# Kernel tuning notes

Hardware: AMD Instinct MI355X
Metric: run time of the kernel (lower is better)

## Reference

```python
import jax, jax.numpy as jnp
import numpy as np
from jax.scipy.special import logsumexp

N, K, D = 131072, 256, 32


def setup_inputs() -> dict:
    key = jax.random.key(0)
    k1, k2, k3 = jax.random.split(key, 3)
    points = jax.random.normal(k1, (N, D), dtype=jnp.float32)
    centers = jax.random.uniform(k2, (K, D), dtype=jnp.float32)
    # well-conditioned inverse-sqrt covariances (original used 15*I; scaled to
    # avoid float32 overflow in sqrt(det(covs_inv)) for D=32)
    covs_inv_sqrt = (0.5 * jnp.broadcast_to(jnp.eye(D, dtype=jnp.float32), (K, D, D))
                     + 0.02 * jax.random.normal(k3, (K, D, D), dtype=jnp.float32))
    weights = jnp.ones((K,), dtype=jnp.float32)
    threshold = jnp.zeros((1,), dtype=jnp.float32)
    return {"points": points, "centers": centers,
            "covs_inv_sqrt": covs_inv_sqrt, "weights": weights,
            "threshold": threshold}


def reference(points, centers, covs_inv_sqrt, weights, threshold):
    # refresh(): equal_clusters=True branch
    w = jnp.abs(weights)
    center_prs = w / (w.sum() + 1e-30)                       # [K]
    covs_inv = jnp.einsum('kde,kfe->kdf', covs_inv_sqrt, covs_inv_sqrt)  # [K,D,D]
    coefs = center_prs * jnp.sqrt(jnp.linalg.det(covs_inv))  # [K]

    # pairwise weighted sqdist: q_ij = (x_i - c_j)^T A_j (x_i - c_j)
    B = covs_inv.reshape(K, D * D)                           # [K, D*D]
    X2 = (points[:, :, None] * points[:, None, :]).reshape(N, D * D)  # [N, D*D]
    t_xAx = X2 @ B.T                                         # [N, K]
    m = jnp.einsum('kde,ke->kd', covs_inv, centers)          # A_j c_j, [K,D]
    t_xAc = points @ m.T                                     # [N, K]
    t_cAc = jnp.einsum('kd,kd->k', m, centers)               # [K]
    d_ij = -0.5 * (t_xAx - 2.0 * t_xAc + t_cAc[None, :])     # [N, K]

    # weighted logsumexp over centers, then subtract threshold
    ll = logsumexp(d_ij, axis=1, b=coefs[None, :])           # [N]
    return ll[:, None] - threshold[0]                        # [N, 1]
```

## Files before the change

kernel.cpp:

```cpp
#include <hip/hip_runtime.h>
#include <math.h>

#define NPTS 131072
#define KCOMP 256
#define DIM 32
#define KF 576
#define NREAL 560
#define PSIF_BYTES 294912
#define WS_NEED (PSIF_BYTES + KCOMP * 4)

typedef __attribute__((ext_vector_type(8))) short short8;
typedef __attribute__((ext_vector_type(16))) float f32x16;

__device__ __forceinline__ unsigned short f2bf(float v) {
    unsigned u = __float_as_uint(v);
    u += 0x7fffu + ((u >> 16) & 1u);
    return (unsigned short)(u >> 16);
}

__device__ __forceinline__ unsigned pkbf(float lo, float hi) {
#if __has_builtin(__builtin_amdgcn_perm)
    const unsigned a = __float_as_uint(hi) + 0x8000u;
    const unsigned b = __float_as_uint(lo) + 0x8000u;
    return __builtin_amdgcn_perm(a, b, 0x07060302u);
#else
    return (unsigned)f2bf(lo) | ((unsigned)f2bf(hi) << 16);
#endif
}

__device__ __forceinline__ void dma16(const uint4* g, uint4* s) {
    __builtin_amdgcn_global_load_lds(
        (const __attribute__((address_space(1))) void*)g,
        (__attribute__((address_space(3))) void*)s, 16, 0, 0);
}

__device__ __forceinline__ void barrier_lds_only() {
    asm volatile("s_waitcnt lgkmcnt(0)\ns_barrier" ::: "memory");
}

constexpr int PfxT(int d) { return 32 * d - (d * (d - 1)) / 2; }
constexpr int rowT(int p) { int d = 0; while (d < 31 && PfxT(d + 1) <= p) ++d; return d; }
constexpr int colT(int p) { return rowT(p) + (p - PfxT(rowT(p))); }

template<int P, int J>
__device__ __forceinline__ float genOne(const float (&x)[DIM]) {
    constexpr int p = P + J;
    if constexpr (p >= NREAL) {
        return 0.f;
    } else if constexpr (p >= 528) {
        return x[p - 528];
    } else {
        constexpr int d = rowT(p);
        constexpr int f = colT(p);
        static_assert(d >= 0 && d < 32 && f >= d && f < 32, "bad feature map");
        return x[d] * x[f];
    }
}

__global__ __launch_bounds__(256) void gmm_pre(
    const float* __restrict__ S,
    const float* __restrict__ centers,
    const float* __restrict__ weights,
    unsigned short* __restrict__ PsiF,
    float* __restrict__ kc2)
{
    __shared__ float Sl[DIM][DIM + 1];
    __shared__ float As[DIM][DIM + 1];
    __shared__ float cl[DIM], ml[DIM];
    __shared__ float red[256];

    const int k = blockIdx.x, tid = threadIdx.x;

    for (int idx = tid; idx < DIM * DIM; idx += 256)
        Sl[idx >> 5][idx & 31] = S[(size_t)k * DIM * DIM + idx];
    if (tid < DIM) cl[tid] = centers[k * DIM + tid];
    __syncthreads();

    for (int idx = tid; idx < DIM * DIM; idx += 256) {
        const int d = idx >> 5, f = idx & 31;
        float a = 0.f;
#pragma unroll
        for (int e = 0; e < DIM; ++e) a = fmaf(Sl[d][e], Sl[f][e], a);
        As[d][f] = a;
    }
    __syncthreads();

    if (tid < DIM) {
        float mv = 0.f;
#pragma unroll
        for (int f = 0; f < DIM; ++f) mv = fmaf(As[tid][f], cl[f], mv);
        ml[tid] = mv;
    }
    __syncthreads();

    for (int p = tid; p < NREAL; p += 256) {
        float val;
        if (p < 528) {
            int d = 0, pr = 0;
            while (pr + (32 - d) <= p) { pr += (32 - d); ++d; }
            const int f = d + (p - pr);
            val = (f == d) ? -0.5f * As[d][d] : -As[d][f];
        } else {
            val = ml[p - 528];
        }
        const int c = p >> 6, kk = p & 63;
        const int s = kk >> 4, qq = (kk >> 3) & 1, j = kk & 7;
        const int ct = k >> 5, ll = qq * 32 + (k & 31);
        const int g = c * 2048 + (s * 8 + ct) * 64 + ll;
        PsiF[(size_t)g * 8 + j] = f2bf(val);
    }

    red[tid] = fabsf(weights[tid]);
    __syncthreads();
    for (int off = 128; off > 0; off >>= 1) {
        if (tid < off) red[tid] += red[tid + off];
        __syncthreads();
    }
    const float wsum = red[0];

    for (int j = 0; j < DIM - 1; ++j) {
        const float inv = 1.0f / As[j][j];
        for (int idx = tid; idx < DIM * DIM; idx += 256) {
            const int r = idx >> 5, c = idx & 31;
            if (r > j && c > j)
                As[r][c] = fmaf(-As[r][j] * inv, As[j][c], As[r][c]);
        }
        __syncthreads();
    }

    if (tid < DIM) red[tid] = __logf(As[tid][tid]);
    __syncthreads();
    if (tid == 0) {
        float sl = 0.f;
        for (int j = 0; j < DIM; ++j) sl += red[j];
        float cac = 0.f;
        for (int d2 = 0; d2 < DIM; ++d2) cac = fmaf(ml[d2], cl[d2], cac);
        kc2[k] = __logf(fabsf(weights[k])) - __logf(wsum + 1e-30f)
               + 0.5f * sl - 0.5f * cac;
    }
}

template<int P>
__device__ __forceinline__ void genQuad(const float (&x)[DIM], float* v) {
    v[0] = genOne<P, 0>(x);
    v[1] = genOne<P, 1>(x);
    v[2] = genOne<P, 2>(x);
    v[3] = genOne<P, 3>(x);
}

template<int C, int SS>
__device__ __forceinline__ void genSite(const float (&x)[DIM], uint4* sA4,
                                        int rbg, int r32) {
    float v[8];
    genQuad<C * 64 + SS * 8>(x, v);
    genQuad<C * 64 + SS * 8 + 4>(x, v + 4);
    uint4 u;
    u.x = pkbf(v[0], v[1]);
    u.y = pkbf(v[2], v[3]);
    u.z = pkbf(v[4], v[5]);
    u.w = pkbf(v[6], v[7]);
    sA4[(SS >> 1) * 256 + rbg * 64 + (SS & 1) * 32 + r32] = u;
}

template<int C>
__device__ __forceinline__ void doChunk(const float (&x)[DIM],
    uint4* sA4, uint4* sB4, const uint4* __restrict__ PsiF4,
    f32x16 (&acc0)[4], f32x16 (&acc1)[4],
    int l, int w, int q, int rbg, int r32, int r0, int c0)
{
    constexpr int NS  = (C < 8) ? 4 : 3;
    constexpr int NSn = (C < 7) ? 4 : ((C == 7) ? 3 : 0);

    if constexpr (C > 0) barrier_lds_only();
    if (q == 0) {
        genSite<C, 0>(x, sA4, rbg, r32);
        genSite<C, 2>(x, sA4, rbg, r32);
        if constexpr (NS >= 3) genSite<C, 4>(x, sA4, rbg, r32);
        if constexpr (NS == 4) genSite<C, 6>(x, sA4, rbg, r32);
    } else {
        genSite<C, 1>(x, sA4, rbg, r32);
        genSite<C, 3>(x, sA4, rbg, r32);
        if constexpr (NS >= 3) genSite<C, 5>(x, sA4, rbg, r32);
        if constexpr (NS == 4) genSite<C, 7>(x, sA4, rbg, r32);
    }
    __syncthreads();

    if constexpr (NSn > 0) {
        const uint4* src = PsiF4 + (C + 1) * 2048 + w * 64 + l;
        uint4* dst = sB4 + ((C + 1) & 1) * 2048 + w * 64 + l;
#pragma unroll
        for (int i = 0; i < NSn * 2; ++i) dma16(src + i * 256, dst + i * 256);
    }

    const uint4* bb = sB4 + (C & 1) * 2048;
#pragma unroll
    for (int s = 0; s < NS; ++s) {
        short8 a0 = __builtin_bit_cast(short8, sA4[(s * 4 + r0) * 64 + l]);
        short8 a1 = __builtin_bit_cast(short8, sA4[(s * 4 + r0 + 1) * 64 + l]);
#pragma unroll
        for (int j = 0; j < 4; ++j) {
            short8 b = __builtin_bit_cast(short8, bb[(s * 8 + c0 + j) * 64 + l]);
            acc0[j] = __builtin_amdgcn_mfma_f32_32x32x16_bf16(a0, b, acc0[j], 0, 0, 0);
            acc1[j] = __builtin_amdgcn_mfma_f32_32x32x16_bf16(a1, b, acc1[j], 0, 0, 0);
        }
    }
}

__device__ __forceinline__ void epiHalf(const f32x16 (&acc)[4], const float (&kcv)[4],
    int rblock, int l, int whalf, float (*sM)[2], float (*sS)[2])
{
#pragma unroll
    for (int rg = 0; rg < 16; ++rg) {
        float vals[4], m = -INFINITY;
#pragma unroll
        for (int j = 0; j < 4; ++j) { vals[j] = acc[j][rg] + kcv[j]; m = fmaxf(m, vals[j]); }
#pragma unroll
        for (int mask = 1; mask < 32; mask <<= 1) m = fmaxf(m, __shfl_xor(m, mask, 64));
        float sv = 0.f;
#pragma unroll
        for (int j = 0; j < 4; ++j) sv += __expf(vals[j] - m);
#pragma unroll
        for (int mask = 1; mask < 32; mask <<= 1) sv += __shfl_xor(sv, mask, 64);
        if ((l & 31) == 0) {
            const int R = rblock * 32 + (rg & 3) + 8 * (rg >> 2) + 4 * (l >> 5);
            sM[R][whalf] = m; sS[R][whalf] = sv;
        }
    }
}

__global__ __launch_bounds__(256, 2) void gmm_mfma(
    const float* __restrict__ points,
    const unsigned short* __restrict__ PsiF,
    const float* __restrict__ kc2,
    const float* __restrict__ thr,
    float* __restrict__ out)
{
    __shared__ uint4 sA4[1024];
    __shared__ uint4 sB4[4096];
    float (*sM)[2] = (float (*)[2])sA4;
    float (*sS)[2] = (float (*)[2])(sA4 + 64);

    const int t = threadIdx.x;
    const int w = t >> 6, l = t & 63;
    const int row = t & 127, q = t >> 7;
    const int rbg = row >> 5, r32 = row & 31;
    const int r0 = (w >> 1) * 2, c0 = (w & 1) * 4;

    const uint4* PsiF4 = (const uint4*)PsiF;

    {
        const uint4* src = PsiF4 + w * 64 + l;
        uint4* dst = sB4 + w * 64 + l;
#pragma unroll
        for (int i = 0; i < 8; ++i) dma16(src + i * 256, dst + i * 256);
    }

    float x[DIM];
    const float4* px = (const float4*)(points + ((size_t)blockIdx.x * 128 + row) * DIM);
#pragma unroll
    for (int j2 = 0; j2 < 8; ++j2) {
        float4 v = px[j2];
        x[4 * j2 + 0] = v.x; x[4 * j2 + 1] = v.y;
        x[4 * j2 + 2] = v.z; x[4 * j2 + 3] = v.w;
    }

    f32x16 acc0[4], acc1[4];
#pragma unroll
    for (int j = 0; j < 4; ++j)
#pragma unroll
        for (int r = 0; r < 16; ++r) { acc0[j][r] = 0.f; acc1[j][r] = 0.f; }

    doChunk<0>(x, sA4, sB4, PsiF4, acc0, acc1, l, w, q, rbg, r32, r0, c0);
    doChunk<1>(x, sA4, sB4, PsiF4, acc0, acc1, l, w, q, rbg, r32, r0, c0);
    doChunk<2>(x, sA4, sB4, PsiF4, acc0, acc1, l, w, q, rbg, r32, r0, c0);
    doChunk<3>(x, sA4, sB4, PsiF4, acc0, acc1, l, w, q, rbg, r32, r0, c0);
    doChunk<4>(x, sA4, sB4, PsiF4, acc0, acc1, l, w, q, rbg, r32, r0, c0);
    doChunk<5>(x, sA4, sB4, PsiF4, acc0, acc1, l, w, q, rbg, r32, r0, c0);
    doChunk<6>(x, sA4, sB4, PsiF4, acc0, acc1, l, w, q, rbg, r32, r0, c0);
    doChunk<7>(x, sA4, sB4, PsiF4, acc0, acc1, l, w, q, rbg, r32, r0, c0);
    doChunk<8>(x, sA4, sB4, PsiF4, acc0, acc1, l, w, q, rbg, r32, r0, c0);

    float kcv[4];
#pragma unroll
    for (int j = 0; j < 4; ++j) kcv[j] = kc2[(c0 + j) * 32 + (l & 31)];

    __syncthreads();
    epiHalf(acc0, kcv, r0,     l, w & 1, sM, sS);
    epiHalf(acc1, kcv, r0 + 1, l, w & 1, sM, sS);
    __syncthreads();

    if (t < 128) {
        const float m0 = sM[t][0], m1 = sM[t][1];
        const float M = fmaxf(m0, m1);
        const float Sv = sS[t][0] * __expf(m0 - M) + sS[t][1] * __expf(m1 - M);
        out[(size_t)blockIdx.x * 128 + t] = M + __logf(Sv) - thr[0];
    }
}

extern "C" void kernel_launch(void* const* d_in, const int* in_sizes, int n_in,
                              void* d_out, int out_size, void* d_ws, size_t ws_size,
                              hipStream_t stream) {
    const float* points  = (const float*)d_in[0];
    const float* centers = (const float*)d_in[1];
    const float* covs    = (const float*)d_in[2];
    const float* weights = (const float*)d_in[3];
    const float* thr     = (const float*)d_in[4];
    float* out = (float*)d_out;

    unsigned short* PsiF = (unsigned short*)d_ws;
    float* kc2 = (float*)((char*)d_ws + PSIF_BYTES);

    gmm_pre<<<KCOMP, 256, 0, stream>>>(covs, centers, weights, PsiF, kc2);
    gmm_mfma<<<NPTS / 128, 256, 0, stream>>>(points, PsiF, kc2, thr, out);
}
```

Measured before the change: 148.1 us.

## Double-buffer A features and halve K-chunk size to overlap generation with MFMA

The K dimension is split into 18 chunks of 32 features instead of 9 of 64. Both the generated bf16 feature tile (A) and the DMA'd PsiF tile (B) are now double-buffered, so the next chunk's features are generated while the current chunk's MFMAs run, leaving one barrier per chunk. This aims to hide the feature-generation VALU work behind matrix work and cuts the B shared-memory footprint, at the cost of twice as many barriers and shorter DMA prefetch lead time.

Result: no change. 147.3 us (-0.5%).

```diff
diff --git a/kernel.cpp b/kernel.cpp
--- a/kernel.cpp
+++ b/kernel.cpp
@@ -4,8 +4,8 @@
 #define NPTS 131072
 #define KCOMP 256
 #define DIM 32
-#define KF 576
 #define NREAL 560
+#define NCH 18
 #define PSIF_BYTES 294912
 #define WS_NEED (PSIF_BYTES + KCOMP * 4)
 
@@ -32,10 +32,6 @@
     __builtin_amdgcn_global_load_lds(
         (const __attribute__((address_space(1))) void*)g,
         (__attribute__((address_space(3))) void*)s, 16, 0, 0);
-}
-
-__device__ __forceinline__ void barrier_lds_only() {
-    asm volatile("s_waitcnt lgkmcnt(0)\ns_barrier" ::: "memory");
 }
 
 constexpr int PfxT(int d) { return 32 * d - (d * (d - 1)) / 2; }
@@ -148,18 +144,31 @@
     v[3] = genOne<P, 3>(x);
 }
 
-template<int C, int SS>
-__device__ __forceinline__ void genSite(const float (&x)[DIM], uint4* sA4,
+template<int CH, int SS>
+__device__ __forceinline__ void genSite(const float (&x)[DIM], uint4* base,
                                         int rbg, int r32) {
     float v[8];
-    genQuad<C * 64 + SS * 8>(x, v);
-    genQuad<C * 64 + SS * 8 + 4>(x, v + 4);
+    genQuad<CH * 32 + SS * 8>(x, v);
+    genQuad<CH * 32 + SS * 8 + 4>(x, v + 4);
     uint4 u;
     u.x = pkbf(v[0], v[1]);
     u.y = pkbf(v[2], v[3]);
     u.z = pkbf(v[4], v[5]);
     u.w = pkbf(v[6], v[7]);
-    sA4[(SS >> 1) * 256 + rbg * 64 + (SS & 1) * 32 + r32] = u;
+    base[(SS >> 1) * 256 + rbg * 64 + (SS & 1) * 32 + r32] = u;
+}
+
+template<int CH>
+__device__ __forceinline__ void genChunk(const float (&x)[DIM], uint4* sA4,
+                                         int q, int rbg, int r32) {
+    uint4* base = sA4 + (CH & 1) * 512;
+    if (q == 0) {
+        genSite<CH, 0>(x, base, rbg, r32);
+        if constexpr (CH < 17) genSite<CH, 2>(x, base, rbg, r32);
+    } else {
+        genSite<CH, 1>(x, base, rbg, r32);
+        if constexpr (CH < 17) genSite<CH, 3>(x, base, rbg, r32);
+    }
 }
 
 template<int C>
@@ -168,35 +177,24 @@
     f32x16 (&acc0)[4], f32x16 (&acc1)[4],
     int l, int w, int q, int rbg, int r32, int r0, int c0)
 {
-    constexpr int NS  = (C < 8) ? 4 : 3;
-    constexpr int NSn = (C < 7) ? 4 : ((C == 7) ? 3 : 0);
-
-    if constexpr (C > 0) barrier_lds_only();
-    if (q == 0) {
-        genSite<C, 0>(x, sA4, rbg, r32);
-        genSite<C, 2>(x, sA4, rbg, r32);
-        if constexpr (NS >= 3) genSite<C, 4>(x, sA4, rbg, r32);
-        if constexpr (NS == 4) genSite<C, 6>(x, sA4, rbg, r32);
-    } else {
-        genSite<C, 1>(x, sA4, rbg, r32);
-        genSite<C, 3>(x, sA4, rbg, r32);
-        if constexpr (NS >= 3) genSite<C, 5>(x, sA4, rbg, r32);
-        if constexpr (NS == 4) genSite<C, 7>(x, sA4, rbg, r32);
-    }
-    __syncthreads();
-
-    if constexpr (NSn > 0) {
-        const uint4* src = PsiF4 + (C + 1) * 2048 + w * 64 + l;
-        uint4* dst = sB4 + ((C + 1) & 1) * 2048 + w * 64 + l;
-#pragma unroll
-        for (int i = 0; i < NSn * 2; ++i) dma16(src + i * 256, dst + i * 256);
-    }
-
-    const uint4* bb = sB4 + (C & 1) * 2048;
+
+    if constexpr (C + 1 < NCH) {
+        constexpr int NI = (C + 1 == 17) ? 2 : 4;
+        const uint4* src = PsiF4 + (C + 1) * 1024 + w * 64 + l;
+        uint4* dst = sB4 + ((C + 1) & 1) * 1024 + w * 64 + l;
+#pragma unroll
+        for (int i = 0; i < NI; ++i) dma16(src + i * 256, dst + i * 256);
+    }
+
+    if constexpr (C + 1 < NCH) genChunk<C + 1>(x, sA4, q, rbg, r32);
+
+    constexpr int NS = (C < 17) ? 2 : 1;
+    const uint4* aa = sA4 + (C & 1) * 512;
+    const uint4* bb = sB4 + (C & 1) * 1024;
 #pragma unroll
     for (int s = 0; s < NS; ++s) {
-        short8 a0 = __builtin_bit_cast(short8, sA4[(s * 4 + r0) * 64 + l]);
-        short8 a1 = __builtin_bit_cast(short8, sA4[(s * 4 + r0 + 1) * 64 + l]);
+        short8 a0 = __builtin_bit_cast(short8, aa[(s * 4 + r0) * 64 + l]);
+        short8 a1 = __builtin_bit_cast(short8, aa[(s * 4 + r0 + 1) * 64 + l]);
 #pragma unroll
         for (int j = 0; j < 4; ++j) {
             short8 b = __builtin_bit_cast(short8, bb[(s * 8 + c0 + j) * 64 + l]);
@@ -204,6 +202,8 @@
             acc1[j] = __builtin_amdgcn_mfma_f32_32x32x16_bf16(a1, b, acc1[j], 0, 0, 0);
         }
     }
+
+    __syncthreads();
 }
 
 __device__ __forceinline__ void epiHalf(const f32x16 (&acc)[4], const float (&kcv)[4],
@@ -236,7 +236,7 @@
     float* __restrict__ out)
 {
     __shared__ uint4 sA4[1024];
-    __shared__ uint4 sB4[4096];
+    __shared__ uint4 sB4[2048];
     float (*sM)[2] = (float (*)[2])sA4;
     float (*sS)[2] = (float (*)[2])(sA4 + 64);
 
@@ -252,7 +252,7 @@
         const uint4* src = PsiF4 + w * 64 + l;
         uint4* dst = sB4 + w * 64 + l;
 #pragma unroll
-        for (int i = 0; i < 8; ++i) dma16(src + i * 256, dst + i * 256);
+        for (int i = 0; i < 4; ++i) dma16(src + i * 256, dst + i * 256);
     }
 
     float x[DIM];
@@ -269,6 +269,9 @@
     for (int j = 0; j < 4; ++j)
 #pragma unroll
         for (int r = 0; r < 16; ++r) { acc0[j][r] = 0.f; acc1[j][r] = 0.f; }
+
+    genChunk<0>(x, sA4, q, rbg, r32);
+    __syncthreads();
 
     doChunk<0>(x, sA4, sB4, PsiF4, acc0, acc1, l, w, q, rbg, r32, r0, c0);
     doChunk<1>(x, sA4, sB4, PsiF4, acc0, acc1, l, w, q, rbg, r32, r0, c0);
@@ -279,12 +282,20 @@
     doChunk<6>(x, sA4, sB4, PsiF4, acc0, acc1, l, w, q, rbg, r32, r0, c0);
     doChunk<7>(x, sA4, sB4, PsiF4, acc0, acc1, l, w, q, rbg, r32, r0, c0);
     doChunk<8>(x, sA4, sB4, PsiF4, acc0, acc1, l, w, q, rbg, r32, r0, c0);
+    doChunk<9>(x, sA4, sB4, PsiF4, acc0, acc1, l, w, q, rbg, r32, r0, c0);
+    doChunk<10>(x, sA4, sB4, PsiF4, acc0, acc1, l, w, q, rbg, r32, r0, c0);
+    doChunk<11>(x, sA4, sB4, PsiF4, acc0, acc1, l, w, q, rbg, r32, r0, c0);
+    doChunk<12>(x, sA4, sB4, PsiF4, acc0, acc1, l, w, q, rbg, r32, r0, c0);
+    doChunk<13>(x, sA4, sB4, PsiF4, acc0, acc1, l, w, q, rbg, r32, r0, c0);
+    doChunk<14>(x, sA4, sB4, PsiF4, acc0, acc1, l, w, q, rbg, r32, r0, c0);
+    doChunk<15>(x, sA4, sB4, PsiF4, acc0, acc1, l, w, q, rbg, r32, r0, c0);
+    doChunk<16>(x, sA4, sB4, PsiF4, acc0, acc1, l, w, q, rbg, r32, r0, c0);
+    doChunk<17>(x, sA4, sB4, PsiF4, acc0, acc1, l, w, q, rbg, r32, r0, c0);
 
     float kcv[4];
 #pragma unroll
     for (int j = 0; j < 4; ++j) kcv[j] = kc2[(c0 + j) * 32 + (l & 31)];
 
-    __syncthreads();
     epiHalf(acc0, kcv, r0,     l, w & 1, sM, sS);
     epiHalf(acc1, kcv, r0 + 1, l, w & 1, sM, sS);
     __syncthreads();
```
